# Kernel tuning notes

Measured on AMD Instinct MI355X. Metric: run time of the kernel, lower is better.

## Reference

```python
import jax, jax.numpy as jnp
import numpy as np

# Config matching init_kwargs
N, C, H, W = 16, 256, 56, 56
O, KS, STRIDE, PAD = 512, 3, 1, 1
TABLE_SIZE, M_AUG = 16, 5
BUCKET = O // TABLE_SIZE            # fixed bucket size (32) for static shapes
SPAN = KS * KS * C                  # kernel_span = 2304


def _np_hash(a, v):
    # hf: abs(floor(a . v)) mod table_size  (matches fmod_ then abs_ on the torch side)
    return int(abs(np.floor(np.dot(a, v)))) % TABLE_SIZE


def setup_inputs() -> dict:
    rng = np.random.default_rng(0)
    stdv = 1.0 / np.sqrt(SPAN)
    kernels = rng.uniform(-stdv, stdv, (O, SPAN)).astype(np.float32)
    a = rng.standard_normal(SPAN + M_AUG).astype(np.float32)
    # _build_alsh_table: hash each kernel row via P(x,m) = concat(x, ||x||^2,...,||x||^(2^m))
    buckets = [[] for _ in range(TABLE_SIZE)]
    for r in range(O):
        k = kernels[r]
        nrm = float(np.linalg.norm(k))
        powers = np.array([nrm ** (2 ** (i + 1)) for i in range(M_AUG)], dtype=np.float32)
        buckets[_np_hash(a, np.concatenate([k, powers]))].append(r)
    # pack into equal-size buckets (overflow spills to the next bucket with space)
    # so that the selected-row count is static and jit-compatible.
    table = np.zeros((TABLE_SIZE, BUCKET), dtype=np.int32)
    fill = [0] * TABLE_SIZE
    overflow = []
    for b in range(TABLE_SIZE):
        for r in buckets[b]:
            if fill[b] < BUCKET:
                table[b, fill[b]] = r
                fill[b] += 1
            else:
                overflow.append(r)
    for r in overflow:
        for b in range(TABLE_SIZE):
            if fill[b] < BUCKET:
                table[b, fill[b]] = r
                fill[b] += 1
                break
    x = jax.random.normal(jax.random.key(0), (N, C, H, W), dtype=jnp.float32)
    return {"x": x, "kernels": jnp.asarray(kernels), "a": jnp.asarray(a),
            "table": jnp.asarray(table)}


def reference(x, kernels, a, table):
    h2 = (H - KS + 2 * PAD) // STRIDE + 1
    w2 = (W - KS + 2 * PAD) // STRIDE + 1
    # im2col: (kh*kw, N, C, h2, w2); stride=1 so plain slices suffice
    xp = jnp.pad(x, ((0, 0), (0, 0), (PAD, PAD), (PAD, PAD)))
    patches = jnp.stack([xp[:, :, i:i + h2, j:j + w2]
                         for i in range(KS) for j in range(KS)])
    # layout (kh, kw, C) along rows to match kernels.view(O, -1)
    pm = patches.transpose(0, 2, 1, 3, 4).reshape(SPAN, -1)  # (SPAN, N*h2*w2)
    # query: torch.rand(5).long() == 0, so the 5 "random" columns are all column 0
    col0 = pm[:, 0]
    unit = col0 / jnp.linalg.norm(col0)
    q = jnp.concatenate([unit, jnp.full((M_AUG,), 0.5, dtype=unit.dtype)])  # Q(x,m)
    idx = (jnp.abs(jnp.floor(jnp.dot(a, q))).astype(jnp.int32)) % TABLE_SIZE
    rows = table[idx]                       # (BUCKET,) selected kernel rows
    sub = kernels[rows] @ pm                # (BUCKET, N*h2*w2) subset matmul
    out = sub * (O / BUCKET)                # out /= rows.size/O
    out = out.reshape(BUCKET, N, h2 * w2).transpose(1, 0, 2)
    return out.reshape(N, BUCKET, h2, w2)
```

## Files before the change

### kernel.cpp

```cpp
#include <hip/hip_runtime.h>
#include <stdint.h>

#define C_IN 256
#define HW   56
#define HW2  3136
#define SPAN 2304
#define TS   16
#define BKT  32

typedef __attribute__((ext_vector_type(8)))  short short8;
typedef __attribute__((ext_vector_type(4)))  float f32x4;
typedef __attribute__((ext_vector_type(16))) float f32x16;
typedef float f32x4u __attribute__((ext_vector_type(4), aligned(4)));


__global__ void hash_rows_kernel(const float* __restrict__ x,
                                 const float* __restrict__ a,
                                 const int*   __restrict__ table,
                                 int*         __restrict__ rows_out) {
    __shared__ float rd[256];
    __shared__ float rn[256];
    const int t = threadIdx.x;
    float dv = 0.f, nq = 0.f;
    for (int k = t; k < SPAN; k += 256) {
        const int p = k >> 8;
        const int c = k & 255;
        const int i = p / 3, j = p % 3;
        float v = 0.f;
        if (i >= 1 && j >= 1) v = x[c * HW2 + (i - 1) * HW + (j - 1)];
        dv += a[k] * v;
        nq += v * v;
    }
    rd[t] = dv; rn[t] = nq;
    __syncthreads();
    for (int s = 128; s > 0; s >>= 1) {
        if (t < s) { rd[t] += rd[t + s]; rn[t] += rn[t + s]; }
        __syncthreads();
    }
    if (t == 0) {
        const float nrm = sqrtf(rn[0]);
        const float sv  = rd[0] / nrm
                        + 0.5f * (a[SPAN] + a[SPAN+1] + a[SPAN+2] + a[SPAN+3] + a[SPAN+4]);
        const int idx = ((int)fabsf(floorf(sv))) % TS;
        #pragma unroll
        for (int b = 0; b < BKT; ++b) rows_out[b] = table[idx * BKT + b];
    }
}

__global__ void build_wpack_kernel(const float* __restrict__ kernels,
                                   const int*   __restrict__ rows,
                                   unsigned short* __restrict__ wp) {
    const int idx   = blockIdx.x * 256 + threadIdx.x;
    const int j     = idx & 7;
    const int l     = (idx >> 3) & 63;
    const int Q     = idx >> 9;
    const int ccb   = Q / 18;
    const int rem   = Q % 18;
    const int p     = rem >> 1;
    const int ch16  = rem & 1;
    const int brow  = l & 31;
    const int khalf = l >> 5;
    const int k     = p * 256 + ccb * 32 + ch16 * 16 + khalf * 8 + j;
    const int row   = rows[brow];
    const float v = kernels[(size_t)row * SPAN + k] * 16.0f;
    unsigned u = __builtin_bit_cast(unsigned, v);
    u = (u + 0x7fffu + ((u >> 16) & 1u)) >> 16;
    wp[idx] = (unsigned short)u;
}

__global__ __launch_bounds__(512, 4)
void alsh_mfma_kernel(const float* __restrict__ x,
                      const unsigned short* __restrict__ wp,
                      float* __restrict__ out) {
    __shared__ float red[4 * 1024];

    const int b  = blockIdx.x;
    const int ct = (b & 7) * 196 + (b >> 3);

    const int t     = threadIdx.x;
    const int lane  = t & 63;
    const int wid   = t >> 6;
    const int ccb   = wid;
    const int col   = lane & 31;
    const int khalf = lane >> 5;
    const int s0    = ct * 32;
    const int n     = s0 / HW2;
    const int s0img = s0 - n * HW2;
    const int sl    = s0img + col;
    const int h     = sl / HW;
    const int w     = sl - h * HW;
    const float* xn = x + (size_t)n * (C_IN * HW2);
    const short8* wpv = (const short8*)wp;

    f32x16 acc = {0.f,0.f,0.f,0.f, 0.f,0.f,0.f,0.f, 0.f,0.f,0.f,0.f, 0.f,0.f,0.f,0.f};

    const int cc = ccb * 32;
    #pragma unroll
    for (int dd = 0; dd < 3; ++dd) {
        const int di     = dd - 1;
        const int rowpos = sl + di * HW;
        const int posm   = rowpos - 1;
        const int pc     = posm < 0 ? 0 : (posm > HW2 - 4 ? HW2 - 4 : posm);
        const bool shifted = (pc != posm);
        const int ih = h + di;

        #pragma unroll
        for (int ch16 = 0; ch16 < 2; ++ch16) {
            f32x4 V[8];
            #pragma unroll
            for (int j = 0; j < 8; ++j) {
                const int ch = cc + ch16 * 16 + khalf * 8 + j;
                V[j] = *(const f32x4u*)(xn + (size_t)ch * HW2 + pc);
            }

            #pragma unroll
            for (int dd2 = 0; dd2 < 3; ++dd2) {
                const int dj = dd2 - 1;
                const int iw = w + dj;
                const bool ok = ((unsigned)ih < (unsigned)HW) & ((unsigned)iw < (unsigned)HW);
                const int voff = rowpos + dj;

                short8 bf;
                #pragma unroll
                for (int j = 0; j < 8; ++j) {
                    float v = V[j][dd2];
                    if (shifted) {
                        const int vc = voff < 0 ? 0 : (voff > HW2 - 1 ? HW2 - 1 : voff);
                        v = xn[(size_t)(cc + ch16 * 16 + khalf * 8 + j) * HW2 + vc];
                    }
                    v = ok ? v : 0.f;
                    const unsigned u = __builtin_bit_cast(unsigned, v);
                    bf[j] = (short)((u + 0x8000u) >> 16);
                }

                const int Q = ccb * 18 + (dd * 3 + dd2) * 2 + ch16;
                const short8 a = wpv[Q * 64 + lane];
                acc = __builtin_amdgcn_mfma_f32_32x32x16_bf16(a, bf, acc, 0, 0, 0);
            }
        }
    }

    const int base = (wid & 3) * 1024;
    if (wid < 4) {
        #pragma unroll
        for (int i2 = 0; i2 < 16; ++i2) {
            const int b0 = (i2 & 3) + 8 * (i2 >> 2) + 4 * khalf;
            red[base + b0 * 32 + col] = acc[i2];
        }
    }
    __syncthreads();
    if (wid >= 4) {
        #pragma unroll
        for (int i2 = 0; i2 < 16; ++i2) {
            const int b0 = (i2 & 3) + 8 * (i2 >> 2) + 4 * khalf;
            red[base + b0 * 32 + col] += acc[i2];
        }
    }
    __syncthreads();

    float* on = out + (size_t)n * (BKT * HW2) + s0img;
    #pragma unroll
    for (int e = 0; e < 2; ++e) {
        const int elem = e * 512 + t;
        const float s = red[elem] + red[1024 + elem] + red[2048 + elem] + red[3072 + elem];
        const int b0 = elem >> 5;
        const int c  = elem & 31;
        on[(size_t)b0 * HW2 + c] = s;
    }
}

extern "C" void kernel_launch(void* const* d_in, const int* in_sizes, int n_in,
                              void* d_out, int out_size, void* d_ws, size_t ws_size,
                              hipStream_t stream) {
    const float* x       = (const float*)d_in[0];
    const float* kernels = (const float*)d_in[1];
    const float* a       = (const float*)d_in[2];
    const int*   table   = (const int*)d_in[3];
    float* out = (float*)d_out;
    int*   rows = (int*)d_ws;
    unsigned short* wpack = (unsigned short*)((char*)d_ws + 512);

    hipLaunchKernelGGL(hash_rows_kernel, dim3(1), dim3(256), 0, stream,
                       x, a, table, rows);
    hipLaunchKernelGGL(build_wpack_kernel, dim3(288), dim3(256), 0, stream,
                       kernels, rows, wpack);
    hipLaunchKernelGGL(alsh_mfma_kernel, dim3(1568), dim3(512), 0, stream,
                       x, wpack, out);
}
```

Baseline: 49.77 us.

## Stage input row windows into LDS via direct global-to-LDS loads

Each wave now copies a 32-channel by 40-position window of the input row into its own LDS region with global_load_lds. The im2col B fragments are then read from LDS. This replaces the per-lane unaligned vector global loads and the scalar fallback loads used at image edges. The six weight fragments for each kernel row offset are also hoisted into registers before the barrier. The cost is two block-wide barriers per row offset, and the LDS footprint grows to 40KB, which may limit occupancy.

```diff
diff --git a/kernel.cpp b/kernel.cpp
--- a/kernel.cpp
+++ b/kernel.cpp
@@ -11,7 +11,13 @@
 typedef __attribute__((ext_vector_type(8)))  short short8;
 typedef __attribute__((ext_vector_type(4)))  float f32x4;
 typedef __attribute__((ext_vector_type(16))) float f32x16;
-typedef float f32x4u __attribute__((ext_vector_type(4), aligned(4)));
+
+__device__ __forceinline__ void gload_lds4(const float* g, float* l) {
+    __builtin_amdgcn_global_load_lds(
+        (const __attribute__((address_space(1))) void*)g,
+        (__attribute__((address_space(3))) void*)l,
+        4, 0, 0);
+}
 
 
 __global__ void hash_rows_kernel(const float* __restrict__ x,
@@ -72,7 +78,7 @@
 void alsh_mfma_kernel(const float* __restrict__ x,
                       const unsigned short* __restrict__ wp,
                       float* __restrict__ out) {
-    __shared__ float red[4 * 1024];
+    __shared__ float lds[10240];
 
     const int b  = blockIdx.x;
     const int ct = (b & 7) * 196 + (b >> 3);
@@ -92,54 +98,62 @@
     const float* xn = x + (size_t)n * (C_IN * HW2);
     const short8* wpv = (const short8*)wp;
 
+    float* wstage = lds + wid * 1280;
+
     f32x16 acc = {0.f,0.f,0.f,0.f, 0.f,0.f,0.f,0.f, 0.f,0.f,0.f,0.f, 0.f,0.f,0.f,0.f};
-
     const int cc = ccb * 32;
+
     #pragma unroll
     for (int dd = 0; dd < 3; ++dd) {
-        const int di     = dd - 1;
+        const int di = dd - 1;
+        int ws = s0img + di * HW - 4;
+        ws = ws < 0 ? 0 : (ws > HW2 - 40 ? HW2 - 40 : ws);
+        const float* gsrc = xn + (size_t)cc * HW2 + ws;
+
+        #pragma unroll
+        for (int i = 0; i < 20; ++i) {
+            const int e   = i * 64 + lane;
+            const int chl = e / 40;
+            const int pos = e - chl * 40;
+            gload_lds4(gsrc + (size_t)chl * HW2 + pos, wstage + i * 64);
+        }
+
+        short8 A6[6];
+        #pragma unroll
+        for (int c2 = 0; c2 < 6; ++c2)
+            A6[c2] = wpv[(ccb * 18 + dd * 6 + c2) * 64 + lane];
+
+        __syncthreads();
+
+        const int ih     = h + di;
         const int rowpos = sl + di * HW;
-        const int posm   = rowpos - 1;
-        const int pc     = posm < 0 ? 0 : (posm > HW2 - 4 ? HW2 - 4 : posm);
-        const bool shifted = (pc != posm);
-        const int ih = h + di;
-
         #pragma unroll
         for (int ch16 = 0; ch16 < 2; ++ch16) {
-            f32x4 V[8];
-            #pragma unroll
-            for (int j = 0; j < 8; ++j) {
-                const int ch = cc + ch16 * 16 + khalf * 8 + j;
-                V[j] = *(const f32x4u*)(xn + (size_t)ch * HW2 + pc);
-            }
-
             #pragma unroll
             for (int dd2 = 0; dd2 < 3; ++dd2) {
                 const int dj = dd2 - 1;
                 const int iw = w + dj;
                 const bool ok = ((unsigned)ih < (unsigned)HW) & ((unsigned)iw < (unsigned)HW);
-                const int voff = rowpos + dj;
+                int p = rowpos + dj - ws;
+                p = ok ? p : 0;
+                const float* rb = wstage + (ch16 * 16 + khalf * 8) * 40 + p;
 
                 short8 bf;
                 #pragma unroll
                 for (int j = 0; j < 8; ++j) {
-                    float v = V[j][dd2];
-                    if (shifted) {
-                        const int vc = voff < 0 ? 0 : (voff > HW2 - 1 ? HW2 - 1 : voff);
-                        v = xn[(size_t)(cc + ch16 * 16 + khalf * 8 + j) * HW2 + vc];
-                    }
+                    float v = rb[j * 40];
                     v = ok ? v : 0.f;
                     const unsigned u = __builtin_bit_cast(unsigned, v);
                     bf[j] = (short)((u + 0x8000u) >> 16);
                 }
 
-                const int Q = ccb * 18 + (dd * 3 + dd2) * 2 + ch16;
-                const short8 a = wpv[Q * 64 + lane];
-                acc = __builtin_amdgcn_mfma_f32_32x32x16_bf16(a, bf, acc, 0, 0, 0);
+                acc = __builtin_amdgcn_mfma_f32_32x32x16_bf16(A6[dd2 * 2 + ch16], bf, acc, 0, 0, 0);
             }
         }
-    }
-
+        __syncthreads();
+    }
+
+    float* red = lds;
     const int base = (wid & 3) * 1024;
     if (wid < 4) {
         #pragma unroll
@@ -163,9 +177,7 @@
     for (int e = 0; e < 2; ++e) {
         const int elem = e * 512 + t;
         const float s = red[elem] + red[1024 + elem] + red[2048 + elem] + red[3072 + elem];
-        const int b0 = elem >> 5;
-        const int c  = elem & 31;
-        on[(size_t)b0 * HW2 + c] = s;
+        on[(size_t)(elem >> 5) * HW2 + (elem & 31)] = s;
     }
 }
 
```

Result: slower. 91.12 us (+83.1%).
